# Performance work log

Measured on AMD Instinct MI355X. Metric: run time of the kernel, lower is better.

The kernel has to match this reference:

```python
import jax, jax.numpy as jnp
import numpy as np

D_MODEL = 2048
N_HEADS = 16
D_HEAD = D_MODEL // N_HEADS
B, S = 2, 2048
EPS = 1e-5


def setup_inputs() -> dict:
    key = jax.random.key(0)
    ks = jax.random.split(key, 10)
    sd = 1.0 / np.sqrt(D_MODEL)
    inp = {
        "X": jax.random.normal(ks[0], (B, S, D_MODEL), dtype=jnp.float32),
        "ln_g": jnp.ones((D_MODEL,), jnp.float32),
        "ln_b": jnp.zeros((D_MODEL,), jnp.float32),
        "Wq": jax.random.uniform(ks[1], (D_MODEL, D_MODEL), jnp.float32, -sd, sd),
        "bq": jax.random.uniform(ks[2], (D_MODEL,), jnp.float32, -sd, sd),
        "Wk": jax.random.uniform(ks[3], (D_MODEL, D_MODEL), jnp.float32, -sd, sd),
        "bk": jax.random.uniform(ks[4], (D_MODEL,), jnp.float32, -sd, sd),
        "Wv": jax.random.uniform(ks[5], (D_MODEL, D_MODEL), jnp.float32, -sd, sd),
        "bv": jax.random.uniform(ks[6], (D_MODEL,), jnp.float32, -sd, sd),
        "Wo": jax.random.uniform(ks[7], (D_MODEL, D_MODEL), jnp.float32, -sd, sd),
        "bo": jax.random.uniform(ks[8], (D_MODEL,), jnp.float32, -sd, sd),
    }
    return inp


def _mhsa(X, ln_g, ln_b, Wq, bq, Wk, bk, Wv, bv, Wo, bo):
    n_ctx = X.shape[-2]
    # pre-LayerNorm
    mu = jnp.mean(X, axis=-1, keepdims=True)
    var = jnp.mean(jnp.square(X - mu), axis=-1, keepdims=True)
    Xn = (X - mu) * jax.lax.rsqrt(var + EPS) * ln_g + ln_b
    # projections (torch Linear stores [out,in]; here W is [in,out])
    def split_heads(t):  # [B,S,D] -> [B,H,S,Dh]
        return t.reshape(t.shape[:-1] + (N_HEADS, D_HEAD)).swapaxes(-2, -3)
    Q = split_heads(Xn @ Wq + bq)
    K = split_heads(Xn @ Wk + bk)
    V = split_heads(Xn @ Wv + bv)
    scores = jnp.einsum("bhqd,bhkd->bhqk", Q, K) / jnp.sqrt(jnp.float32(D_HEAD))
    causal = jnp.tril(jnp.ones((n_ctx, n_ctx), dtype=bool))
    scores = jnp.where(causal, scores, jnp.float32(-jnp.inf))
    A = jax.nn.softmax(scores, axis=-1)
    AV = jnp.einsum("bhqk,bhkd->bhqd", A, V)
    AV = AV.swapaxes(-2, -3).reshape(X.shape[:-1] + (D_MODEL,))
    return AV @ Wo + bo


def reference(X, ln_g, ln_b, Wq, bq, Wk, bk, Wv, bv, Wo, bo):
    return _mhsa(X, ln_g, ln_b, Wq, bq, Wk, bk, Wv, bv, Wo, bo)
```

## Files before the change

kernel.cpp:

```cpp
#include <hip/hip_runtime.h>
#include <cstdint>

constexpr int kDM = 2048;
constexpr int kNH = 16;
constexpr int kDH = 128;
constexpr int kS  = 2048;
constexpr int kM  = 4096;

typedef __bf16 bf16x8 __attribute__((ext_vector_type(8)));
typedef float  f32x4  __attribute__((ext_vector_type(4)));

__device__ __forceinline__ unsigned short f2bf(float f) {
    union { float f; unsigned u; } v; v.f = f;
    unsigned u = v.u;
    u += 0x7fffu + ((u >> 16) & 1u);
    return (unsigned short)(u >> 16);
}
__device__ __forceinline__ float bf2f(unsigned short b) {
    union { unsigned u; float f; } v; v.u = ((unsigned)b) << 16;
    return v.f;
}
__device__ __forceinline__ float fast_exp2(float x) {
#if __has_builtin(__builtin_amdgcn_exp2f)
    return __builtin_amdgcn_exp2f(x);
#else
    return exp2f(x);
#endif
}
__device__ __forceinline__ void load_lds16(const void* g, void* l) {
    auto gp = (__attribute__((address_space(1))) unsigned int*)(uintptr_t)g;
    auto lp = (__attribute__((address_space(3))) unsigned int*)(uintptr_t)l;
    __builtin_amdgcn_global_load_lds(gp, lp, 16, 0, 0);
}

__global__ __launch_bounds__(256) void ln_kernel(const float* __restrict__ X,
        const float* __restrict__ g, const float* __restrict__ b,
        unsigned short* __restrict__ Xn) {
    const int row = blockIdx.x;
    const float* xr = X + (size_t)row * kDM;
    const float4 v0 = ((const float4*)xr)[threadIdx.x];
    const float4 v1 = ((const float4*)xr)[threadIdx.x + 256];
    float s  = v0.x + v0.y + v0.z + v0.w + v1.x + v1.y + v1.z + v1.w;
    float sq = v0.x*v0.x + v0.y*v0.y + v0.z*v0.z + v0.w*v0.w
             + v1.x*v1.x + v1.y*v1.y + v1.z*v1.z + v1.w*v1.w;
    #pragma unroll
    for (int m = 1; m < 64; m <<= 1) { s += __shfl_xor(s, m); sq += __shfl_xor(sq, m); }
    __shared__ float ls[4], lq[4];
    if ((threadIdx.x & 63) == 0) { ls[threadIdx.x >> 6] = s; lq[threadIdx.x >> 6] = sq; }
    __syncthreads();
    s  = ls[0] + ls[1] + ls[2] + ls[3];
    sq = lq[0] + lq[1] + lq[2] + lq[3];
    const float mu   = s * (1.0f / kDM);
    const float rstd = rsqrtf(sq * (1.0f / kDM) - mu * mu + 1e-5f);
    unsigned short* xo = Xn + (size_t)row * kDM;
    {
        const float4 gg = ((const float4*)g)[threadIdx.x];
        const float4 bb = ((const float4*)b)[threadIdx.x];
        ushort4 o;
        o.x = f2bf((v0.x - mu) * rstd * gg.x + bb.x);
        o.y = f2bf((v0.y - mu) * rstd * gg.y + bb.y);
        o.z = f2bf((v0.z - mu) * rstd * gg.z + bb.z);
        o.w = f2bf((v0.w - mu) * rstd * gg.w + bb.w);
        ((ushort4*)xo)[threadIdx.x] = o;
    }
    {
        const float4 gg = ((const float4*)g)[threadIdx.x + 256];
        const float4 bb = ((const float4*)b)[threadIdx.x + 256];
        ushort4 o;
        o.x = f2bf((v1.x - mu) * rstd * gg.x + bb.x);
        o.y = f2bf((v1.y - mu) * rstd * gg.y + bb.y);
        o.z = f2bf((v1.z - mu) * rstd * gg.z + bb.z);
        o.w = f2bf((v1.w - mu) * rstd * gg.w + bb.w);
        ((ushort4*)xo)[threadIdx.x + 256] = o;
    }
}

__global__ __launch_bounds__(256) void wt_kernel(
        const float* __restrict__ W0, const float* __restrict__ W1,
        const float* __restrict__ W2, const float* __restrict__ W3,
        unsigned short* __restrict__ T0, unsigned short* __restrict__ T1,
        unsigned short* __restrict__ T2, unsigned short* __restrict__ T3) {
    const float* W; unsigned short* T;
    switch (blockIdx.z) {
        case 0:  W = W0; T = T0; break;
        case 1:  W = W1; T = T1; break;
        case 2:  W = W2; T = T2; break;
        default: W = W3; T = T3; break;
    }
    __shared__ float tile[32][33];
    const int tx = threadIdx.x & 31, ty = threadIdx.x >> 5;
    const int r0 = blockIdx.y * 32, c0 = blockIdx.x * 32;
    #pragma unroll
    for (int i = 0; i < 4; ++i)
        tile[ty + i * 8][tx] = W[(size_t)(r0 + ty + i * 8) * kDM + c0 + tx];
    __syncthreads();
    #pragma unroll
    for (int i = 0; i < 4; ++i)
        T[(size_t)(c0 + ty + i * 8) * kDM + r0 + tx] = f2bf(tile[tx][ty + i * 8]);
}

__global__ __launch_bounds__(256) void bias_pack(const float* __restrict__ bq,
        const float* __restrict__ bk, const float* __restrict__ bv,
        float* __restrict__ o) {
    const int i = blockIdx.x * 256 + threadIdx.x;
    o[i] = (i < 2048) ? bq[i] : ((i < 4096) ? bk[i - 2048] : bv[i - 4096]);
}

__global__ __launch_bounds__(256) void vtr_kernel(const unsigned short* __restrict__ Vin,
                                                  unsigned short* __restrict__ Vout) {
    __shared__ __align__(16) unsigned short tile[64 * 72];
    const int bhz = blockIdx.z;
    const int s0 = blockIdx.x * 64, d0 = blockIdx.y * 64;
    const int t = threadIdx.x;
    const unsigned short* src = Vin + ((size_t)bhz * kS + s0) * kDH + d0;
    #pragma unroll
    for (int i = 0; i < 2; ++i) {
        const int r = (t >> 3) + 32 * i;
        const int g = t & 7;
        *(uint4*)(tile + r * 72 + g * 8) = *(const uint4*)(src + (size_t)r * kDH + g * 8);
    }
    __syncthreads();
    unsigned short* dst = Vout + ((size_t)bhz * kDH + d0) * kS + s0;
    #pragma unroll
    for (int i = 0; i < 2; ++i) {
        const int d = (t >> 3) + 32 * i;
        const int sg = t & 7;
        union { unsigned short u[8]; uint4 v; } o;
        #pragma unroll
        for (int j = 0; j < 8; ++j)
            o.u[j] = tile[(sg * 8 + j) * 72 + d];
        *(uint4*)(dst + (size_t)d * kS + sg * 8) = o.v;
    }
}

__global__ __launch_bounds__(256) void gemm_kernel(
        const unsigned short* __restrict__ A, const unsigned short* __restrict__ Bt,
        const float* __restrict__ bias, void* __restrict__ C0, void* __restrict__ C1,
        void* __restrict__ C2, const float scale0, const int fp32out) {
    __shared__ __align__(16) unsigned short ldsA[2][128 * 32];
    __shared__ __align__(16) unsigned short ldsB[2][128 * 32];
    const int m0 = blockIdx.x * 128, n0 = blockIdx.y * 128;
    const int tid = threadIdx.x, lane = tid & 63, w = tid >> 6;
    const int wm = (w >> 1) * 64, wn = (w & 1) * 64;
    const int quad = lane >> 4, l15 = lane & 15;
    f32x4 acc[4][4] = {};
    const int srow = lane >> 2, scol = (lane & 3) * 8;
    for (int k0 = 0; k0 < kDM; k0 += 64) {
        __syncthreads();
        #pragma unroll
        for (int sub = 0; sub < 2; ++sub) {
            #pragma unroll
            for (int i = 0; i < 2; ++i) {
                const int c = w + i * 4;
                const int row = c * 16 + srow;
                const int kc = k0 + sub * 32 + scol;
                load_lds16(A  + (size_t)(m0 + row) * kDM + kc, &ldsA[sub][c * 512]);
                load_lds16(Bt + (size_t)(n0 + row) * kDM + kc, &ldsB[sub][c * 512]);
            }
        }
        __syncthreads();
        #pragma unroll
        for (int sub = 0; sub < 2; ++sub) {
            bf16x8 af[4], bfr[4];
            #pragma unroll
            for (int mt = 0; mt < 4; ++mt)
                af[mt] = *(const bf16x8*)(&ldsA[sub][(wm + mt * 16 + l15) * 32 + quad * 8]);
            #pragma unroll
            for (int nt = 0; nt < 4; ++nt)
                bfr[nt] = *(const bf16x8*)(&ldsB[sub][(wn + nt * 16 + l15) * 32 + quad * 8]);
            #pragma unroll
            for (int mt = 0; mt < 4; ++mt)
                #pragma unroll
                for (int nt = 0; nt < 4; ++nt)
                    acc[mt][nt] = __builtin_amdgcn_mfma_f32_16x16x32_bf16(af[mt], bfr[nt], acc[mt][nt], 0, 0, 0);
        }
    }
    const int proj = n0 >> 11;
    void* Cb = (proj == 0) ? C0 : ((proj == 1) ? C1 : C2);
    const float scl = (proj == 0) ? scale0 : 1.0f;
    #pragma unroll
    for (int mt = 0; mt < 4; ++mt) {
        #pragma unroll
        for (int nt = 0; nt < 4; ++nt) {
            const int ng = n0 + wn + nt * 16 + l15;
            const float bv = bias[ng];
            const int col = ng & 2047;
            const int h = col >> 7, dh = col & 127;
            #pragma unroll
            for (int r = 0; r < 4; ++r) {
                const int mg = m0 + wm + mt * 16 + quad * 4 + r;
                const float val = (acc[mt][nt][r] + bv) * scl;
                if (fp32out) {
                    ((float*)Cb)[(size_t)mg * kDM + ng] = val;
                } else {
                    const int bb = mg >> 11, ss = mg & 2047;
                    ((unsigned short*)Cb)[((size_t)(bb * kNH + h) * kS + ss) * kDH + dh] = f2bf(val);
                }
            }
        }
    }
}

__global__ __launch_bounds__(256, 2) void attn_kernel(
        const unsigned short* __restrict__ Q, const unsigned short* __restrict__ Kk,
        const unsigned short* __restrict__ Vt, unsigned short* __restrict__ AV) {
    __shared__ __align__(16) unsigned short ldsK[64 * 128];
    __shared__ __align__(16) unsigned short ldsV[128 * 64];
    __shared__ __align__(16) unsigned short ldsP[4 * 16 * 64];
    const int bh = blockIdx.x, pr = blockIdx.y;
    const unsigned short* Qb = Q  + (size_t)bh * kS * kDH;
    const unsigned short* Kb = Kk + (size_t)bh * kS * kDH;
    const unsigned short* Vb = Vt + (size_t)bh * kDH * kS;
    const int tid = threadIdx.x, lane = tid & 63, w = tid >> 6;
    const int quad = lane >> 4, l15 = lane & 15;
    int kSrc[4], vSrc[4], ldst[4];
    #pragma unroll
    for (int i = 0; i < 4; ++i) {
        const int c = w * 4 + i;
        const int rK = c * 4 + (lane >> 4);
        const int gK = (lane & 15) ^ (rK & 15);
        kSrc[i] = rK * kDH + gK * 8;
        const int dV = c * 8 + (lane >> 3);
        const int gV = (lane & 7) ^ (dV & 7);
        vSrc[i] = dV * kS + gV * 8;
        ldst[i] = c * 512;
    }
    unsigned short* pw = ldsP + w * 1024;
    const int pswz = 2 * (l15 & 7);
    const int bb = bh >> 4, h = bh & 15;
    for (int half = 0; half < 2; ++half) {
        const int qt = half ? (31 - pr) : pr;
        const int qrow0 = qt * 64 + w * 16;
        bf16x8 qf[4];
        #pragma unroll
        for (int kk = 0; kk < 4; ++kk)
            qf[kk] = *(const bf16x8*)(Qb + (size_t)(qrow0 + l15) * kDH + kk * 32 + quad * 8);
        f32x4 accO[8] = {};
        float mrun = -3.0e38f, lrun = 0.0f;
        for (int kt = 0; kt <= qt; ++kt) {
            __syncthreads();
            #pragma unroll
            for (int i = 0; i < 4; ++i) {
                load_lds16(Kb + (size_t)kt * (64 * kDH) + kSrc[i], ldsK + ldst[i]);
                load_lds16(Vb + kt * 64 + vSrc[i], ldsV + ldst[i]);
            }
            __syncthreads();
            f32x4 accS[4] = {};
            #pragma unroll
            for (int kk = 0; kk < 4; ++kk) {
                bf16x8 kf[4];
                #pragma unroll
                for (int mt = 0; mt < 4; ++mt)
                    kf[mt] = *(const bf16x8*)(ldsK + (mt * 16 + l15) * 128 + (((kk * 4 + quad) ^ l15) << 3));
                #pragma unroll
                for (int mt = 0; mt < 4; ++mt)
                    accS[mt] = __builtin_amdgcn_mfma_f32_16x16x32_bf16(kf[mt], qf[kk], accS[mt], 0, 0, 0);
            }
            if (kt == qt) {
                const int ql = w * 16 + l15;
                #pragma unroll
                for (int mt = 0; mt < 4; ++mt)
                    #pragma unroll
                    for (int r = 0; r < 4; ++r)
                        if (mt * 16 + quad * 4 + r > ql) accS[mt][r] = -3.0e38f;
            }
            float mx = accS[0][0];
            #pragma unroll
            for (int mt = 0; mt < 4; ++mt)
                #pragma unroll
                for (int r = 0; r < 4; ++r) mx = fmaxf(mx, accS[mt][r]);
            mx = fmaxf(mx, __shfl_xor(mx, 16));
            mx = fmaxf(mx, __shfl_xor(mx, 32));
            const float mnew = fmaxf(mrun, mx);
            const float al = fast_exp2(mrun - mnew);
            float rs = 0.f;
            #pragma unroll
            for (int mt = 0; mt < 4; ++mt) {
                ushort4 pk;
                unsigned short* pe = (unsigned short*)&pk;
                #pragma unroll
                for (int r = 0; r < 4; ++r) {
                    const float p = fast_exp2(accS[mt][r] - mnew);
                    const unsigned short pb = f2bf(p);
                    pe[r] = pb;
                    rs += bf2f(pb);
                }
                *(ushort4*)(pw + l15 * 64 + (((mt * 4 + quad) ^ pswz) << 2)) = pk;
            }
            rs += __shfl_xor(rs, 16);
            rs += __shfl_xor(rs, 32);
            lrun = lrun * al + rs;
            mrun = mnew;
            float albr[4];
            #pragma unroll
            for (int r = 0; r < 4; ++r)
                albr[r] = __shfl(al, (lane & 48) | (quad << 2) | r);
            #pragma unroll
            for (int dt = 0; dt < 8; ++dt)
                #pragma unroll
                for (int r = 0; r < 4; ++r)
                    accO[dt][r] *= albr[r];
            asm volatile("s_waitcnt lgkmcnt(0)" ::: "memory");
            #pragma unroll
            for (int kk = 0; kk < 2; ++kk) {
                const bf16x8 pa = *(const bf16x8*)(pw + l15 * 64 + (((kk * 8 + quad * 2) ^ pswz) << 2));
                #pragma unroll
                for (int dt = 0; dt < 8; ++dt) {
                    const bf16x8 vf = *(const bf16x8*)(ldsV + (dt * 16 + l15) * 64 + (((kk * 4 + quad) ^ (l15 & 7)) << 3));
                    accO[dt] = __builtin_amdgcn_mfma_f32_16x16x32_bf16(pa, vf, accO[dt], 0, 0, 0);
                }
            }
        }
        float linv[4];
        #pragma unroll
        for (int r = 0; r < 4; ++r)
            linv[r] = __shfl(lrun, (lane & 48) | (quad << 2) | r);
        #pragma unroll
        for (int r = 0; r < 4; ++r) {
            const float inv = 1.0f / linv[r];
            unsigned short* orow = AV + ((size_t)bb * kS + qrow0 + quad * 4 + r) * kDM + h * kDH;
            #pragma unroll
            for (int dt = 0; dt < 8; ++dt)
                orow[dt * 16 + l15] = f2bf(accO[dt][r] * inv);
        }
    }
}

extern "C" void kernel_launch(void* const* d_in, const int* in_sizes, int n_in,
                              void* d_out, int out_size, void* d_ws, size_t ws_size,
                              hipStream_t stream) {
    const float* X   = (const float*)d_in[0];
    const float* lng = (const float*)d_in[1];
    const float* lnb = (const float*)d_in[2];
    const float* Wq  = (const float*)d_in[3];
    const float* bq  = (const float*)d_in[4];
    const float* Wk  = (const float*)d_in[5];
    const float* bk  = (const float*)d_in[6];
    const float* Wv  = (const float*)d_in[7];
    const float* bv  = (const float*)d_in[8];
    const float* Wo  = (const float*)d_in[9];
    const float* bo  = (const float*)d_in[10];
    float* out = (float*)d_out;

    char* p = (char*)d_ws;
    unsigned short* Xn  = (unsigned short*)p; p += (size_t)kM * kDM * 2;
    unsigned short* Wqt = (unsigned short*)p; p += (size_t)kDM * kDM * 2;
    unsigned short* Wkt = (unsigned short*)p; p += (size_t)kDM * kDM * 2;
    unsigned short* Wvt = (unsigned short*)p; p += (size_t)kDM * kDM * 2;
    unsigned short* Wot = (unsigned short*)p; p += (size_t)kDM * kDM * 2;
    unsigned short* Qb  = (unsigned short*)p; p += (size_t)kM * kDM * 2;
    unsigned short* Kb  = (unsigned short*)p; p += (size_t)kM * kDM * 2;
    unsigned short* Vtb = (unsigned short*)p; p += (size_t)kM * kDM * 2;
    unsigned short* AV  = (unsigned short*)p; p += (size_t)kM * kDM * 2;
    unsigned short* Vtmp = AV;
    float* biasc = (float*)Vtb;

    const float qscale = 0.08838834764831845f * 1.4426950408889634f;

    ln_kernel<<<dim3(kM), dim3(256), 0, stream>>>(X, lng, lnb, Xn);
    wt_kernel<<<dim3(64, 64, 4), dim3(256), 0, stream>>>(Wq, Wk, Wv, Wo, Wqt, Wkt, Wvt, Wot);
    bias_pack<<<dim3(24), dim3(256), 0, stream>>>(bq, bk, bv, biasc);
    gemm_kernel<<<dim3(32, 48), dim3(256), 0, stream>>>(Xn, Wqt, biasc, Qb, Kb, Vtmp, qscale, 0);
    vtr_kernel<<<dim3(32, 2, 32), dim3(256), 0, stream>>>(Vtmp, Vtb);
    attn_kernel<<<dim3(32, 16), dim3(256), 0, stream>>>(Qb, Kb, Vtb, AV);
    gemm_kernel<<<dim3(32, 16), dim3(256), 0, stream>>>(AV, Wot, bo, out, out, out, 1.0f, 1);
}
```

Measured before the change: 391.9 us.

## Enlarge attention query tile to 128 rows with double-buffered K/V loads

```diff
diff --git a/kernel.cpp b/kernel.cpp
--- a/kernel.cpp
+++ b/kernel.cpp
@@ -15,10 +15,6 @@
     unsigned u = v.u;
     u += 0x7fffu + ((u >> 16) & 1u);
     return (unsigned short)(u >> 16);
-}
-__device__ __forceinline__ float bf2f(unsigned short b) {
-    union { unsigned u; float f; } v; v.u = ((unsigned)b) << 16;
-    return v.f;
 }
 __device__ __forceinline__ float fast_exp2(float x) {
 #if __has_builtin(__builtin_amdgcn_exp2f)
@@ -204,15 +200,17 @@
 __global__ __launch_bounds__(256, 2) void attn_kernel(
         const unsigned short* __restrict__ Q, const unsigned short* __restrict__ Kk,
         const unsigned short* __restrict__ Vt, unsigned short* __restrict__ AV) {
-    __shared__ __align__(16) unsigned short ldsK[64 * 128];
-    __shared__ __align__(16) unsigned short ldsV[128 * 64];
-    __shared__ __align__(16) unsigned short ldsP[4 * 16 * 64];
-    const int bh = blockIdx.x, pr = blockIdx.y;
+    __shared__ __align__(16) unsigned short ldsK[2][64 * 128];
+    __shared__ __align__(16) unsigned short ldsV[2][128 * 64];
+    __shared__ __align__(16) unsigned short ldsP[4][32 * 64];
+    const int bh = blockIdx.x;
+    const int qt = (int)gridDim.y - 1 - (int)blockIdx.y;
     const unsigned short* Qb = Q  + (size_t)bh * kS * kDH;
     const unsigned short* Kb = Kk + (size_t)bh * kS * kDH;
     const unsigned short* Vb = Vt + (size_t)bh * kDH * kS;
     const int tid = threadIdx.x, lane = tid & 63, w = tid >> 6;
     const int quad = lane >> 4, l15 = lane & 15;
+    const int wq = qt * 128 + w * 32;
     int kSrc[4], vSrc[4], ldst[4];
     #pragma unroll
     for (int i = 0; i < 4; ++i) {
@@ -225,54 +223,71 @@
         vSrc[i] = dV * kS + gV * 8;
         ldst[i] = c * 512;
     }
-    unsigned short* pw = ldsP + w * 1024;
+    unsigned short* pw = ldsP[w];
     const int pswz = 2 * (l15 & 7);
-    const int bb = bh >> 4, h = bh & 15;
-    for (int half = 0; half < 2; ++half) {
-        const int qt = half ? (31 - pr) : pr;
-        const int qrow0 = qt * 64 + w * 16;
-        bf16x8 qf[4];
+    bf16x8 qf[2][4];
+    #pragma unroll
+    for (int qg = 0; qg < 2; ++qg)
         #pragma unroll
         for (int kk = 0; kk < 4; ++kk)
-            qf[kk] = *(const bf16x8*)(Qb + (size_t)(qrow0 + l15) * kDH + kk * 32 + quad * 8);
-        f32x4 accO[8] = {};
-        float mrun = -3.0e38f, lrun = 0.0f;
-        for (int kt = 0; kt <= qt; ++kt) {
-            __syncthreads();
+            qf[qg][kk] = *(const bf16x8*)(Qb + (size_t)(wq + qg * 16 + l15) * kDH + kk * 32 + quad * 8);
+    f32x4 accO[2][8] = {};
+    float mrun[2] = {-3.0e38f, -3.0e38f}, lrun[2] = {0.f, 0.f};
+    const int nkt = 2 * qt + 2;
+    #pragma unroll
+    for (int i = 0; i < 4; ++i) {
+        load_lds16(Kb + kSrc[i], &ldsK[0][ldst[i]]);
+        load_lds16(Vb + vSrc[i], &ldsV[0][ldst[i]]);
+    }
+    for (int kt = 0; kt < nkt; ++kt) {
+        const int buf = kt & 1;
+        __syncthreads();
+        if (kt + 1 < nkt) {
+            const size_t ko = (size_t)(kt + 1) * (64 * kDH);
+            const int vo = (kt + 1) * 64;
             #pragma unroll
             for (int i = 0; i < 4; ++i) {
-                load_lds16(Kb + (size_t)kt * (64 * kDH) + kSrc[i], ldsK + ldst[i]);
-                load_lds16(Vb + kt * 64 + vSrc[i], ldsV + ldst[i]);
-            }
-            __syncthreads();
-            f32x4 accS[4] = {};
-            #pragma unroll
-            for (int kk = 0; kk < 4; ++kk) {
-                bf16x8 kf[4];
+                load_lds16(Kb + ko + kSrc[i], &ldsK[buf ^ 1][ldst[i]]);
+                load_lds16(Vb + vo + vSrc[i], &ldsV[buf ^ 1][ldst[i]]);
+            }
+        }
+        if (kt * 64 > wq + 31) continue;
+        f32x4 accS[2][4] = {};
+        #pragma unroll
+        for (int kk = 0; kk < 4; ++kk) {
+            bf16x8 kf[4];
+            #pragma unroll
+            for (int mt = 0; mt < 4; ++mt)
+                kf[mt] = *(const bf16x8*)(&ldsK[buf][(mt * 16 + l15) * 128 + (((kk * 4 + quad) ^ l15) << 3)]);
+            #pragma unroll
+            for (int qg = 0; qg < 2; ++qg)
                 #pragma unroll
                 for (int mt = 0; mt < 4; ++mt)
-                    kf[mt] = *(const bf16x8*)(ldsK + (mt * 16 + l15) * 128 + (((kk * 4 + quad) ^ l15) << 3));
-                #pragma unroll
-                for (int mt = 0; mt < 4; ++mt)
-                    accS[mt] = __builtin_amdgcn_mfma_f32_16x16x32_bf16(kf[mt], qf[kk], accS[mt], 0, 0, 0);
-            }
-            if (kt == qt) {
-                const int ql = w * 16 + l15;
+                    accS[qg][mt] = __builtin_amdgcn_mfma_f32_16x16x32_bf16(kf[mt], qf[qg][kk], accS[qg][mt], 0, 0, 0);
+        }
+        if (kt * 64 + 63 > wq) {
+            #pragma unroll
+            for (int qg = 0; qg < 2; ++qg) {
+                const int qgl = wq + qg * 16 + l15;
                 #pragma unroll
                 for (int mt = 0; mt < 4; ++mt)
                     #pragma unroll
                     for (int r = 0; r < 4; ++r)
-                        if (mt * 16 + quad * 4 + r > ql) accS[mt][r] = -3.0e38f;
-            }
-            float mx = accS[0][0];
+                        if (kt * 64 + mt * 16 + quad * 4 + r > qgl) accS[qg][mt][r] = -3.0e38f;
+            }
+        }
+        float al2[2];
+        #pragma unroll
+        for (int qg = 0; qg < 2; ++qg) {
+            float mx = accS[qg][0][0];
             #pragma unroll
             for (int mt = 0; mt < 4; ++mt)
                 #pragma unroll
-                for (int r = 0; r < 4; ++r) mx = fmaxf(mx, accS[mt][r]);
+                for (int r = 0; r < 4; ++r) mx = fmaxf(mx, accS[qg][mt][r]);
             mx = fmaxf(mx, __shfl_xor(mx, 16));
             mx = fmaxf(mx, __shfl_xor(mx, 32));
-            const float mnew = fmaxf(mrun, mx);
-            const float al = fast_exp2(mrun - mnew);
+            const float mnew = fmaxf(mrun[qg], mx);
+            const float al = fast_exp2(mrun[qg] - mnew);
             float rs = 0.f;
             #pragma unroll
             for (int mt = 0; mt < 4; ++mt) {
@@ -280,50 +295,58 @@
                 unsigned short* pe = (unsigned short*)&pk;
                 #pragma unroll
                 for (int r = 0; r < 4; ++r) {
-                    const float p = fast_exp2(accS[mt][r] - mnew);
-                    const unsigned short pb = f2bf(p);
-                    pe[r] = pb;
-                    rs += bf2f(pb);
+                    const float p = fast_exp2(accS[qg][mt][r] - mnew);
+                    pe[r] = f2bf(p);
+                    rs += p;
                 }
-                *(ushort4*)(pw + l15 * 64 + (((mt * 4 + quad) ^ pswz) << 2)) = pk;
+                *(ushort4*)(pw + (qg * 16 + l15) * 64 + (((mt * 4 + quad) ^ pswz) << 2)) = pk;
             }
             rs += __shfl_xor(rs, 16);
             rs += __shfl_xor(rs, 32);
-            lrun = lrun * al + rs;
-            mrun = mnew;
+            lrun[qg] = lrun[qg] * al + rs;
+            mrun[qg] = mnew;
+            al2[qg] = al;
+        }
+        #pragma unroll
+        for (int qg = 0; qg < 2; ++qg) {
             float albr[4];
             #pragma unroll
             for (int r = 0; r < 4; ++r)
-                albr[r] = __shfl(al, (lane & 48) | (quad << 2) | r);
+                albr[r] = __shfl(al2[qg], (lane & 48) | (quad << 2) | r);
             #pragma unroll
             for (int dt = 0; dt < 8; ++dt)
                 #pragma unroll
                 for (int r = 0; r < 4; ++r)
-                    accO[dt][r] *= albr[r];
-            asm volatile("s_waitcnt lgkmcnt(0)" ::: "memory");
-            #pragma unroll
-            for (int kk = 0; kk < 2; ++kk) {
-                const bf16x8 pa = *(const bf16x8*)(pw + l15 * 64 + (((kk * 8 + quad * 2) ^ pswz) << 2));
-                #pragma unroll
-                for (int dt = 0; dt < 8; ++dt) {
-                    const bf16x8 vf = *(const bf16x8*)(ldsV + (dt * 16 + l15) * 64 + (((kk * 4 + quad) ^ (l15 & 7)) << 3));
-                    accO[dt] = __builtin_amdgcn_mfma_f32_16x16x32_bf16(pa, vf, accO[dt], 0, 0, 0);
-                }
-            }
-        }
-        float linv[4];
-        #pragma unroll
-        for (int r = 0; r < 4; ++r)
-            linv[r] = __shfl(lrun, (lane & 48) | (quad << 2) | r);
+                    accO[qg][dt][r] *= albr[r];
+        }
+        asm volatile("s_waitcnt lgkmcnt(0)" ::: "memory");
+        #pragma unroll
+        for (int kk = 0; kk < 2; ++kk) {
+            bf16x8 pa[2];
+            #pragma unroll
+            for (int qg = 0; qg < 2; ++qg)
+                pa[qg] = *(const bf16x8*)(pw + (qg * 16 + l15) * 64 + (((kk * 8 + quad * 2) ^ pswz) << 2));
+            #pragma unroll
+            for (int dt = 0; dt < 8; ++dt) {
+                const bf16x8 vf = *(const bf16x8*)(&ldsV[buf][(dt * 16 + l15) * 64 + (((kk * 4 + quad) ^ (l15 & 7)) << 3)]);
+                #pragma unroll
+                for (int qg = 0; qg < 2; ++qg)
+                    accO[qg][dt] = __builtin_amdgcn_mfma_f32_16x16x32_bf16(pa[qg], vf, accO[qg][dt], 0, 0, 0);
+            }
+        }
+    }
+    const int bb = bh >> 4, h = bh & 15;
+    #pragma unroll
+    for (int qg = 0; qg < 2; ++qg)
         #pragma unroll
         for (int r = 0; r < 4; ++r) {
-            const float inv = 1.0f / linv[r];
-            unsigned short* orow = AV + ((size_t)bb * kS + qrow0 + quad * 4 + r) * kDM + h * kDH;
+            const float li = __shfl(lrun[qg], (lane & 48) | (quad << 2) | r);
+            const float inv = 1.0f / li;
+            unsigned short* orow = AV + ((size_t)bb * kS + wq + qg * 16 + quad * 4 + r) * kDM + h * kDH;
             #pragma unroll
             for (int dt = 0; dt < 8; ++dt)
-                orow[dt * 16 + l15] = f2bf(accO[dt][r] * inv);
-        }
-    }
+                orow[dt * 16 + l15] = f2bf(accO[qg][dt][r] * inv);
+        }
 }
 
 extern "C" void kernel_launch(void* const* d_in, const int* in_sizes, int n_in,
```

Result: slower. 410.2 us (+4.7%).
